# Performance work log

Hardware: AMD Instinct MI355X
Metric: run time of the kernel (lower is better)

Reference implementation:

```python
import jax, jax.numpy as jnp
import numpy as np

B, S, D = 8, 2048, 512


def setup_inputs() -> dict:
    root = jax.random.key(0)
    kq, kk, kv, km = jax.random.split(root, 4)
    query = jax.random.normal(kq, (B, S, D), dtype=jnp.float32)
    key = jax.random.normal(kk, (B, S, D), dtype=jnp.float32)
    value = jax.random.normal(kv, (B, S, D), dtype=jnp.float32)
    # padding mask (batch, key_len): 1 = attend, 0 = masked. Force position 0
    # valid so no causal row is entirely masked (would yield NaN softmax).
    attention_mask = jax.random.randint(km, (B, S), 0, 2, dtype=jnp.int32).at[:, 0].set(1)
    return {"query": query, "key": key, "value": value, "attention_mask": attention_mask}


def reference(query, key, value, attention_mask):
    q_len, k_len = query.shape[1], key.shape[1]
    scale = 1.0 / jnp.sqrt(jnp.asarray(key.shape[-1], dtype=query.dtype))
    # [B, q_len, k_len] scores
    scores = jnp.einsum("bqd,bkd->bqk", query, key) * scale
    # causal (mask_future=True): lower-triangular allowed
    causal = jnp.tril(jnp.ones((q_len, k_len), dtype=bool))
    scores = jnp.where(causal[None, :, :], scores, -jnp.inf)
    # padding mask broadcast over query axis: (B, 1, k_len)
    scores = jnp.where(attention_mask[:, None, :] == 0, -jnp.inf, scores)
    probs = jax.nn.softmax(scores, axis=-1)
    return jnp.einsum("bqk,bkd->bqd", probs, value)
```

## Files before the change

### kernel.cpp

```cpp
#include <hip/hip_runtime.h>
#include <hip/hip_bf16.h>


typedef short bf16x8 __attribute__((ext_vector_type(8)));
typedef short s4v    __attribute__((ext_vector_type(4)));
typedef float f32x4  __attribute__((ext_vector_type(4)));
typedef float f4v    __attribute__((ext_vector_type(4)));
typedef float f2v    __attribute__((ext_vector_type(2)));
typedef unsigned int u32;

#define DEVINL __device__ __forceinline__

constexpr int kS = 2048;
constexpr int kD = 512;
constexpr int kB = 8;
constexpr int QT = 32;
constexpr int KROW = kD + 8;
constexpr float kC = 1.4426950408889634f * 0.044194173824159216f;
constexpr size_t kSlotB = (size_t)64 * kD * 2 + 64 * 4 * 2;

DEVINL float fast_exp2(float x) {
  float r; asm("v_exp_f32 %0, %1" : "=v"(r) : "v"(x)); return r;
}
DEVINL short f2b(float f) {
  return (short)__builtin_bit_cast(unsigned short, __float2bfloat16(f));
}
DEVINL f32x4 mfma16(bf16x8 a, bf16x8 b, f32x4 c) {
  return __builtin_amdgcn_mfma_f32_16x16x32_bf16(a, b, c, 0, 0, 0);
}
DEVINL void gl_lds16(const void* g, void* l) {
  __builtin_amdgcn_global_load_lds(
      (const __attribute__((address_space(1))) u32*)g,
      (__attribute__((address_space(3))) u32*)l, 16, 0, 0);
}
DEVINL float bflo(u32 u) { return __builtin_bit_cast(float, u << 16); }
DEVINL float bfhi(u32 u) { return __builtin_bit_cast(float, u & 0xffff0000u); }

DEVINL int ncOf(int qt, int TT) { return (2 * qt + 2 + TT - 1) / TT; }

__global__ __launch_bounds__(256) void prep(
    const float* __restrict__ K, const float* __restrict__ V,
    short* __restrict__ Kb, short* __restrict__ Vt) {
  __shared__ float Tl[64][65];
  const int blk = blockIdx.x;
  if (blk < 1024) {
    const size_t n4 = (size_t)kB * kS * kD / 4;
    for (size_t i = (size_t)blk * 256 + threadIdx.x; i < n4;
         i += (size_t)1024 * 256) {
      f4v v = *(const f4v*)(K + i * 4);
      s4v o = {f2b(v[0]), f2b(v[1]), f2b(v[2]), f2b(v[3])};
      *(s4v*)(Kb + i * 4) = o;
    }
  } else {
    const int r = blk - 1024;
    const int b = r >> 8, rr = r & 255;
    const int s0 = (rr >> 3) * 64, d0 = (rr & 7) * 64;
    const int t = threadIdx.x;
#pragma unroll
    for (int i = 0; i < 4; ++i) {
      int v = t + i * 256;
      int row = v >> 4, cq = v & 15;
      f4v x = *(const f4v*)(V + ((size_t)(b * kS + s0 + row)) * kD + d0 + cq * 4);
      *(f4v*)&Tl[row][cq * 4] = x;
    }
    __syncthreads();
    const int dd = t >> 2, q = t & 3;
    short out[16];
#pragma unroll
    for (int j = 0; j < 16; ++j) out[j] = f2b(Tl[q * 16 + j][dd]);
    short* dp = Vt + ((size_t)(b * kD + d0 + dd)) * kS + s0 + q * 16;
    *(bf16x8*)dp = *(const bf16x8*)&out[0];
    *(bf16x8*)(dp + 8) = *(const bf16x8*)&out[8];
  }
}

__global__ __launch_bounds__(256, 1) void attn_p1(
    const float* __restrict__ Qp, const short* __restrict__ Kb,
    const short* __restrict__ Vt, const int* __restrict__ Mp,
    float* __restrict__ Op, char* __restrict__ Part, int TT, int NS) {
  __shared__ __align__(16) short Klds[2][32 * 512];
  __shared__ __align__(16) short Vlds[2][128 * 128];
  __shared__ __align__(16) short Plds[4 * 16 * 40];
  __shared__ unsigned char Mlds[kS];

  const int tid = threadIdx.x, lane = tid & 63, w = tid >> 6;
  const int b = blockIdx.x & 7;
  const int NCH = gridDim.x >> 3;
  const int jj = NCH - 1 - (blockIdx.x >> 3);

  int rem = jj, qt = 0, sub = 0;
  for (qt = 0; qt < QT; ++qt) {
    int c = ncOf(qt, TT);
    if (rem < c) { sub = rem; break; }
    rem -= c;
  }
  const int nc = ncOf(qt, TT);
  const int ntl = 2 * qt + 2;
  const int clen = (ntl + nc - 1) / nc;
  const int t0 = sub * clen, t1 = min(ntl, t0 + clen);
  const int qbase = qt * 64;

  for (int i = tid; i < kS; i += 256) Mlds[i] = (unsigned char)Mp[(size_t)b * kS + i];
  __syncthreads();

  const int l15 = lane & 15, lg = lane >> 4;
  const short* kbG = Kb + (size_t)(b * kS) * kD;
  const short* vtG = Vt + (size_t)(b * kD) * kS;

  auto stage = [&](int t, int nb) {
    const int kv0 = t * 32;
    const short* kb = kbG + (size_t)kv0 * kD;
    const short* vt = vtG + kv0;
    const int li = lane & 15, lh = lane >> 4;
#pragma unroll
    for (int r8 = 0; r8 < 8; ++r8) {
      const int row = w * 8 + r8;
      gl_lds16(kb + (size_t)row * kD + ((lane ^ (row & 7)) << 3),
               &Klds[nb][row * 512]);
    }
#pragma unroll
    for (int r8 = 0; r8 < 8; ++r8) {
      const int i = w * 8 + r8;
      const int sr = 4 * i + lh;
      const int logical = li ^ (4 * (i & 1) + lh);
      const int d = sr * 4 + (logical >> 2);
      gl_lds16(vt + (size_t)d * kS + ((logical & 3) << 3), &Vlds[nb][i * 512]);
    }
  };

  stage(t0, 0);

  bf16x8 qa[16];
  {
    const float* qp = Qp + ((size_t)(b * kS) + qbase + w * 16 + l15) * kD + lg * 8;
#pragma unroll
    for (int k = 0; k < 16; ++k) {
      f4v a = *(const f4v*)(qp + k * 32);
      f4v c = *(const f4v*)(qp + k * 32 + 4);
      bf16x8 q8 = {f2b(a[0]), f2b(a[1]), f2b(a[2]), f2b(a[3]),
                   f2b(c[0]), f2b(c[1]), f2b(c[2]), f2b(c[3])};
      qa[k] = q8;
    }
  }

  f32x4 acc[32];
#pragma unroll
  for (int dc = 0; dc < 32; ++dc) acc[dc] = f32x4{0.f, 0.f, 0.f, 0.f};
  float mrow[4] = {-1e30f, -1e30f, -1e30f, -1e30f};
  float lsum[4] = {0.f, 0.f, 0.f, 0.f};

  short* Pl = &Plds[w * 16 * 40];

  const int kx4 = (l15 >> 2) & 1;
  const int kcom = l15 * 512 + ((lg ^ (l15 & 3)) << 3);
  const int kEo = kcom + (kx4 << 5);
  const int kOo = kcom - (kx4 << 5);
  const int vcom = (l15 >> 2) * 128 + ((l15 >> 1) & 1) * 64 + ((lg ^ (l15 >> 2)) << 3);
  const int vEo = vcom + (l15 & 1) * 32;
  const int vOo = vcom + ((l15 & 1) ^ 1) * 32;

  for (int t = t0; t < t1; ++t) {
    const int cur = (t - t0) & 1;
    const int kv0 = t * 32;

    if (t + 1 < t1) {
      stage(t + 1, cur ^ 1);
      asm volatile("s_waitcnt vmcnt(16)" ::: "memory");
    } else {
      asm volatile("s_waitcnt vmcnt(0)" ::: "memory");
    }
    __builtin_amdgcn_s_barrier();
    __builtin_amdgcn_sched_barrier(0);

    const short* KB_ = &Klds[cur][0];
    const short* VB_ = &Vlds[cur][0];
    const short* kpE = KB_ + kEo;
    const short* kpO = KB_ + kOo;

    f32x4 sA = {0.f,0.f,0.f,0.f}, sB = {0.f,0.f,0.f,0.f};
    f32x4 sC = {0.f,0.f,0.f,0.f}, sD = {0.f,0.f,0.f,0.f};
    __builtin_amdgcn_s_setprio(1);
#pragma unroll
    for (int k = 0; k < 16; k += 2) {
      const short* pa = kpE + (k << 5);
      const short* pb = kpO + ((k + 1) << 5);
      bf16x8 b00 = *(const bf16x8*)(pa);
      bf16x8 b10 = *(const bf16x8*)(pa + 16 * 512);
      bf16x8 b01 = *(const bf16x8*)(pb);
      bf16x8 b11 = *(const bf16x8*)(pb + 16 * 512);
      sA = mfma16(qa[k], b00, sA);
      sB = mfma16(qa[k], b10, sB);
      sC = mfma16(qa[k + 1], b01, sC);
      sD = mfma16(qa[k + 1], b11, sD);
    }
    __builtin_amdgcn_s_setprio(0);
    f32x4 s0 = sA + sC;
    f32x4 s1 = sB + sD;

    const int kvg0 = kv0 + l15, kvg1 = kvg0 + 16;
    const int mk0 = Mlds[kvg0], mk1 = Mlds[kvg1];
    const int qrow0 = qbase + w * 16 + lg * 4;
    float rm[4];
#pragma unroll
    for (int jx = 0; jx < 4; ++jx) {
      const int q = qrow0 + jx;
      float x0 = (kvg0 <= q && mk0 != 0) ? s0[jx] : -1e30f;
      float x1 = (kvg1 <= q && mk1 != 0) ? s1[jx] : -1e30f;
      s0[jx] = x0; s1[jx] = x1;
      rm[jx] = fmaxf(x0, x1);
    }
#pragma unroll
    for (int sh = 1; sh <= 8; sh <<= 1) {
#pragma unroll
      for (int jx = 0; jx < 4; ++jx) rm[jx] = fmaxf(rm[jx], __shfl_xor(rm[jx], sh));
    }

    bool need = false;
#pragma unroll
    for (int jx = 0; jx < 4; ++jx) need |= ((rm[jx] - mrow[jx]) * kC > 8.0f);
    if (__any(need)) {
#pragma unroll
      for (int jx = 0; jx < 4; ++jx) {
        float mn = fmaxf(mrow[jx], rm[jx]);
        float corr = fast_exp2((mrow[jx] - mn) * kC);
        mrow[jx] = mn;
        lsum[jx] *= corr;
#pragma unroll
        for (int dc = 0; dc < 32; ++dc) acc[dc][jx] *= corr;
      }
    }

    float ts[4];
#pragma unroll
    for (int jx = 0; jx < 4; ++jx) {
      float p0 = fast_exp2((s0[jx] - mrow[jx]) * kC);
      float p1 = fast_exp2((s1[jx] - mrow[jx]) * kC);
      ts[jx] = p0 + p1;
      Pl[(lg * 4 + jx) * 40 + l15]      = f2b(p0);
      Pl[(lg * 4 + jx) * 40 + 16 + l15] = f2b(p1);
    }
#pragma unroll
    for (int sh = 1; sh <= 8; sh <<= 1) {
#pragma unroll
      for (int jx = 0; jx < 4; ++jx) ts[jx] += __shfl_xor(ts[jx], sh);
    }
#pragma unroll
    for (int jx = 0; jx < 4; ++jx) lsum[jx] += ts[jx];

    bf16x8 pf = *(const bf16x8*)&Pl[l15 * 40 + lg * 8];
    __builtin_amdgcn_s_setprio(1);
#pragma unroll
    for (int dc = 0; dc < 32; dc += 2) {
      bf16x8 vf0 = *(const bf16x8*)(VB_ + vEo + dc * 512);
      bf16x8 vf1 = *(const bf16x8*)(VB_ + vOo + (dc + 1) * 512);
      acc[dc]     = mfma16(pf, vf0, acc[dc]);
      acc[dc + 1] = mfma16(pf, vf1, acc[dc + 1]);
    }
    __builtin_amdgcn_s_setprio(0);

    __builtin_amdgcn_s_barrier();
  }

  if (nc == 1) {
#pragma unroll
    for (int jx = 0; jx < 4; ++jx) {
      const float inv = __builtin_amdgcn_rcpf(lsum[jx]);
      float* op = Op + ((size_t)(b * kS) + qbase + w * 16 + lg * 4 + jx) * kD + l15;
#pragma unroll
      for (int dc = 0; dc < 32; ++dc) op[dc * 16] = acc[dc][jx] * inv;
    }
  } else {
    int sb = 0;
    for (int q = 0; q < qt; ++q) {
      int n2 = ncOf(q, TT);
      if (n2 > 1) sb += n2;
    }
    char* sp = Part + ((size_t)b * NS + sb + sub) * kSlotB;
    short* po = (short*)sp;
    float* pm = (float*)(sp + 65536);
#pragma unroll
    for (int jx = 0; jx < 4; ++jx) {
      const int row = w * 16 + lg * 4 + jx;
#pragma unroll
      for (int dc = 0; dc < 32; ++dc) po[row * kD + dc * 16 + l15] = f2b(acc[dc][jx]);
      if (l15 == 0) { pm[row] = mrow[jx]; pm[64 + row] = lsum[jx]; }
    }
  }
}

__global__ __launch_bounds__(256) void attn_p2(const char* __restrict__ Part,
                                               float* __restrict__ Op,
                                               int TT, int NS) {
  const int bid = blockIdx.x;
  const int b = bid & 7, rg = (bid >> 3) & 7, idx = bid >> 6;
  int seen = 0, qt = 0, nc = 0, sbase = 0, sb = 0;
  for (int q = 0; q < QT; ++q) {
    int n2 = ncOf(q, TT);
    if (n2 > 1) {
      if (seen == idx) { qt = q; nc = n2; sbase = sb; break; }
      seen++;
      sb += n2;
    }
  }
  const int t = threadIdx.x;
  const char* base = Part + ((size_t)b * NS + sbase) * kSlotB;
  const int r0 = rg * 8;
  for (int row = r0; row < r0 + 8; ++row) {
    float M = -1e30f;
    for (int c = 0; c < nc; ++c)
      M = fmaxf(M, *(const float*)(base + c * kSlotB + 65536 + row * 4));
    float lt = 0.f;
    for (int c = 0; c < nc; ++c) {
      float mc = *(const float*)(base + c * kSlotB + 65536 + row * 4);
      float lc = *(const float*)(base + c * kSlotB + 65536 + 256 + row * 4);
      lt += lc * fast_exp2((mc - M) * kC);
    }
    const float inv = 1.0f / lt;
    float a0 = 0.f, a1 = 0.f;
    for (int c = 0; c < nc; ++c) {
      float mc = *(const float*)(base + c * kSlotB + 65536 + row * 4);
      float e = fast_exp2((mc - M) * kC);
      u32 u = *(const u32*)(base + c * kSlotB + ((size_t)row * kD + t * 2) * 2);
      a0 += e * bflo(u);
      a1 += e * bfhi(u);
    }
    f2v o = {a0 * inv, a1 * inv};
    *(f2v*)(Op + ((size_t)(b * kS) + qt * 64 + row) * kD + t * 2) = o;
  }
}

__global__ __launch_bounds__(256) void attn_legacy(
    const float* __restrict__ Qp, const float* __restrict__ Kp,
    const float* __restrict__ Vp, const int* __restrict__ Mp,
    float* __restrict__ Op) {
  __shared__ __align__(16) short Klds[32 * KROW];
  __shared__ __align__(16) short Vlds[32 * kD];
  __shared__ __align__(16) short Plds[4 * 16 * 40];
  __shared__ int Mlds[kS];
  const int tid = threadIdx.x, lane = tid & 63, w = tid >> 6;
  const int bb = blockIdx.x & 7, qt = blockIdx.x >> 3, qb = qt * 64;
  for (int i = tid; i < kS; i += 256) Mlds[i] = Mp[(size_t)bb * kS + i];
  const int l15 = lane & 15, lg = lane >> 4;
  bf16x8 qa[16];
  {
    const float* qp = Qp + ((size_t)bb * kS + qb + w * 16 + l15) * kD + lg * 8;
#pragma unroll
    for (int k = 0; k < 16; ++k) {
      f4v a = *(const f4v*)(qp + k * 32);
      f4v c = *(const f4v*)(qp + k * 32 + 4);
      bf16x8 q8 = {f2b(a[0]), f2b(a[1]), f2b(a[2]), f2b(a[3]),
                   f2b(c[0]), f2b(c[1]), f2b(c[2]), f2b(c[3])};
      qa[k] = q8;
    }
  }
  f32x4 acc[32];
#pragma unroll
  for (int dc = 0; dc < 32; ++dc) acc[dc] = f32x4{0.f, 0.f, 0.f, 0.f};
  float mrow[4] = {-1e30f, -1e30f, -1e30f, -1e30f};
  float lsum[4] = {0.f, 0.f, 0.f, 0.f};
  short* Pl = &Plds[w * 16 * 40];
  const int vphys = ((lg ^ ((lane >> 2) & 3)) * 16);
  const int nt = 2 * qt + 2;
  for (int t = 0; t < nt; ++t) {
    const int kv0 = t * 32;
    __syncthreads();
    {
      const int r = tid >> 3, dg = tid & 7;
      const float* src = Kp + ((size_t)bb * kS + kv0 + r) * kD + dg * 64;
      short* dst = &Klds[r * KROW + dg * 64];
#pragma unroll
      for (int i = 0; i < 16; ++i) {
        f4v v = *(const f4v*)(src + i * 4);
        s4v s = {f2b(v[0]), f2b(v[1]), f2b(v[2]), f2b(v[3])};
        *(s4v*)(dst + i * 4) = s;
      }
    }
    {
      const int kvq = tid & 7, dqi = tid >> 3;
      const float* vbase = Vp + ((size_t)bb * kS + kv0 + kvq * 4) * kD;
#pragma unroll
      for (int it = 0; it < 4; ++it) {
        const int dq = dqi + 32 * it;
        f4v v0 = *(const f4v*)(vbase + 0 * kD + dq * 4);
        f4v v1 = *(const f4v*)(vbase + 1 * kD + dq * 4);
        f4v v2 = *(const f4v*)(vbase + 2 * kD + dq * 4);
        f4v v3 = *(const f4v*)(vbase + 3 * kD + dq * 4);
        const int pch = (((kvq >> 1) ^ (dq & 3)) * 16) + (kvq & 1) * 8;
#pragma unroll
        for (int c = 0; c < 4; ++c) {
          s4v s = {f2b(v0[c]), f2b(v1[c]), f2b(v2[c]), f2b(v3[c])};
          *(s4v*)((char*)Vlds + (dq * 4 + c) * 64 + pch) = s;
        }
      }
    }
    __syncthreads();
    f32x4 sA = {0.f,0.f,0.f,0.f}, sB = {0.f,0.f,0.f,0.f};
    f32x4 sC = {0.f,0.f,0.f,0.f}, sD = {0.f,0.f,0.f,0.f};
    const short* krow0 = &Klds[l15 * KROW + lg * 8];
    const short* krow1 = krow0 + 16 * KROW;
#pragma unroll
    for (int k = 0; k < 16; k += 2) {
      bf16x8 b00 = *(const bf16x8*)(krow0 + k * 32);
      bf16x8 b10 = *(const bf16x8*)(krow1 + k * 32);
      bf16x8 b01 = *(const bf16x8*)(krow0 + (k + 1) * 32);
      bf16x8 b11 = *(const bf16x8*)(krow1 + (k + 1) * 32);
      sA = mfma16(qa[k], b00, sA);
      sB = mfma16(qa[k], b10, sB);
      sC = mfma16(qa[k + 1], b01, sC);
      sD = mfma16(qa[k + 1], b11, sD);
    }
    f32x4 s0 = sA + sC, s1 = sB + sD;
    const int kvg0 = kv0 + l15, kvg1 = kvg0 + 16;
    const int mk0 = Mlds[kvg0], mk1 = Mlds[kvg1];
    const int qrow0 = qb + w * 16 + lg * 4;
    float rm[4];
#pragma unroll
    for (int jx = 0; jx < 4; ++jx) {
      const int q = qrow0 + jx;
      float x0 = (kvg0 <= q && mk0 != 0) ? s0[jx] : -1e30f;
      float x1 = (kvg1 <= q && mk1 != 0) ? s1[jx] : -1e30f;
      s0[jx] = x0; s1[jx] = x1;
      rm[jx] = fmaxf(x0, x1);
    }
#pragma unroll
    for (int sh = 1; sh <= 8; sh <<= 1) {
#pragma unroll
      for (int jx = 0; jx < 4; ++jx) rm[jx] = fmaxf(rm[jx], __shfl_xor(rm[jx], sh));
    }
    bool need = false;
#pragma unroll
    for (int jx = 0; jx < 4; ++jx) need |= ((rm[jx] - mrow[jx]) * kC > 8.0f);
    if (__any(need)) {
#pragma unroll
      for (int jx = 0; jx < 4; ++jx) {
        float mn = fmaxf(mrow[jx], rm[jx]);
        float corr = fast_exp2((mrow[jx] - mn) * kC);
        mrow[jx] = mn;
        lsum[jx] *= corr;
#pragma unroll
        for (int dc = 0; dc < 32; ++dc) acc[dc][jx] *= corr;
      }
    }
    float ts[4];
#pragma unroll
    for (int jx = 0; jx < 4; ++jx) {
      float p0 = fast_exp2((s0[jx] - mrow[jx]) * kC);
      float p1 = fast_exp2((s1[jx] - mrow[jx]) * kC);
      ts[jx] = p0 + p1;
      Pl[(lg * 4 + jx) * 40 + l15]      = f2b(p0);
      Pl[(lg * 4 + jx) * 40 + 16 + l15] = f2b(p1);
    }
#pragma unroll
    for (int sh = 1; sh <= 8; sh <<= 1) {
#pragma unroll
      for (int jx = 0; jx < 4; ++jx) ts[jx] += __shfl_xor(ts[jx], sh);
    }
#pragma unroll
    for (int jx = 0; jx < 4; ++jx) lsum[jx] += ts[jx];
    bf16x8 pf = *(const bf16x8*)&Pl[l15 * 40 + lg * 8];
#pragma unroll
    for (int dc = 0; dc < 32; ++dc) {
      const bf16x8 vf = *(const bf16x8*)((const char*)Vlds + (dc * 16 + l15) * 64 + vphys);
      acc[dc] = mfma16(pf, vf, acc[dc]);
    }
  }
#pragma unroll
  for (int jx = 0; jx < 4; ++jx) {
    const float inv = __builtin_amdgcn_rcpf(lsum[jx]);
    float* op = Op + ((size_t)bb * kS + qb + w * 16 + lg * 4 + jx) * kD + l15;
#pragma unroll
    for (int dc = 0; dc < 32; ++dc) op[dc * 16] = acc[dc][jx] * inv;
  }
}

extern "C" void kernel_launch(void* const* d_in, const int* in_sizes, int n_in,
                              void* d_out, int out_size, void* d_ws, size_t ws_size,
                              hipStream_t stream) {
  const float* Q = (const float*)d_in[0];
  const float* K = (const float*)d_in[1];
  const float* V = (const float*)d_in[2];
  const int*   M = (const int*)d_in[3];
  float* O = (float*)d_out;

  const size_t tens = (size_t)kB * kS * kD;
  const size_t convB = 2 * tens * 2;

  if (ws_size < convB) {
    attn_legacy<<<dim3(256), dim3(256), 0, stream>>>(Q, K, V, M, O);
    return;
  }

  short* Kb = (short*)d_ws;
  short* Vt = Kb + tens;
  char* Part = (char*)d_ws + convB;
  const size_t budget = ws_size - convB;

  int TT = 64;
  {
    const int cands[4] = {16, 22, 33, 48};
    for (int ci = 0; ci < 4; ++ci) {
      int tt = cands[ci], slots = 0;
      for (int q = 0; q < QT; ++q) {
        int nc = (2 * q + 2 + tt - 1) / tt;
        if (nc > 1) slots += nc;
      }
      if ((size_t)kB * slots * kSlotB <= budget) { TT = tt; break; }
    }
  }
  int NS = 0, NCH = 0, nsplit = 0;
  for (int q = 0; q < QT; ++q) {
    int nc = (2 * q + 2 + TT - 1) / TT;
    NCH += nc;
    if (nc > 1) { NS += nc; nsplit++; }
  }

  prep<<<dim3(3072), dim3(256), 0, stream>>>(K, V, Kb, Vt);
  attn_p1<<<dim3(kB * NCH), dim3(256), 0, stream>>>(Q, Kb, Vt, M, O, Part, TT, NS);
  if (nsplit > 0)
    attn_p2<<<dim3(kB * 8 * nsplit), dim3(256), 0, stream>>>(Part, O, TT, NS);
}
```

Measured before the change: 216.2 us.

## Double query tile to 128 rows with 8 waves sharing staged K/V tiles

Each attention block now covers 128 query rows with 512 threads (8 waves), so every staged K/V tile in LDS is reused by twice as many query rows and global-to-LDS traffic per query row is halved. The split-K chunking, partial-slot layout and combine kernel are resized to the new tile. Row max and row sum reductions switch from shuffle loops to DPP row moves. The trade-off is fewer, larger blocks with higher register pressure at two blocks per CU, plus coarser causal load balance.

```diff
diff --git a/kernel.cpp b/kernel.cpp
--- a/kernel.cpp
+++ b/kernel.cpp
@@ -14,10 +14,11 @@
 constexpr int kS = 2048;
 constexpr int kD = 512;
 constexpr int kB = 8;
-constexpr int QT = 32;
+constexpr int QT2 = 16;
 constexpr int KROW = kD + 8;
 constexpr float kC = 1.4426950408889634f * 0.044194173824159216f;
-constexpr size_t kSlotB = (size_t)64 * kD * 2 + 64 * 4 * 2;
+constexpr int kPOff = 128 * kD * 2;
+constexpr size_t kSlot2 = (size_t)kPOff + 128 * 4 * 2;
 
 DEVINL float fast_exp2(float x) {
   float r; asm("v_exp_f32 %0, %1" : "=v"(r) : "v"(x)); return r;
@@ -36,7 +37,29 @@
 DEVINL float bflo(u32 u) { return __builtin_bit_cast(float, u << 16); }
 DEVINL float bfhi(u32 u) { return __builtin_bit_cast(float, u & 0xffff0000u); }
 
-DEVINL int ncOf(int qt, int TT) { return (2 * qt + 2 + TT - 1) / TT; }
+template <int CTRL>
+DEVINL float mvdpp(float x) {
+  return __builtin_bit_cast(float,
+      __builtin_amdgcn_mov_dpp(__builtin_bit_cast(int, x), CTRL, 0xf, 0xf, false));
+}
+DEVINL float rowmax16(float x) {
+  x = fmaxf(x, mvdpp<0x128>(x));
+  x = fmaxf(x, mvdpp<0x124>(x));
+  x = fmaxf(x, mvdpp<0x122>(x));
+  x = fmaxf(x, mvdpp<0x121>(x));
+  return x;
+}
+DEVINL float rowsum16(float x) {
+  x += mvdpp<0x128>(x);
+  x += mvdpp<0x124>(x);
+  x += mvdpp<0x122>(x);
+  x += mvdpp<0x121>(x);
+  return x;
+}
+
+__host__ __device__ __forceinline__ int nc2(int q, int TT) {
+  return (4 * q + 4 + TT - 1) / TT;
+}
 
 __global__ __launch_bounds__(256) void prep(
     const float* __restrict__ K, const float* __restrict__ V,
@@ -74,13 +97,13 @@
   }
 }
 
-__global__ __launch_bounds__(256, 1) void attn_p1(
+__global__ __launch_bounds__(512, 2) void attn_p1(
     const float* __restrict__ Qp, const short* __restrict__ Kb,
     const short* __restrict__ Vt, const int* __restrict__ Mp,
     float* __restrict__ Op, char* __restrict__ Part, int TT, int NS) {
   __shared__ __align__(16) short Klds[2][32 * 512];
   __shared__ __align__(16) short Vlds[2][128 * 128];
-  __shared__ __align__(16) short Plds[4 * 16 * 40];
+  __shared__ __align__(16) short Plds[8 * 16 * 40];
   __shared__ unsigned char Mlds[kS];
 
   const int tid = threadIdx.x, lane = tid & 63, w = tid >> 6;
@@ -89,18 +112,18 @@
   const int jj = NCH - 1 - (blockIdx.x >> 3);
 
   int rem = jj, qt = 0, sub = 0;
-  for (qt = 0; qt < QT; ++qt) {
-    int c = ncOf(qt, TT);
+  for (qt = 0; qt < QT2; ++qt) {
+    int c = nc2(qt, TT);
     if (rem < c) { sub = rem; break; }
     rem -= c;
   }
-  const int nc = ncOf(qt, TT);
-  const int ntl = 2 * qt + 2;
+  const int nc = nc2(qt, TT);
+  const int ntl = 4 * qt + 4;
   const int clen = (ntl + nc - 1) / nc;
   const int t0 = sub * clen, t1 = min(ntl, t0 + clen);
-  const int qbase = qt * 64;
-
-  for (int i = tid; i < kS; i += 256) Mlds[i] = (unsigned char)Mp[(size_t)b * kS + i];
+  const int qbase = qt * 128;
+
+  for (int i = tid; i < kS; i += 512) Mlds[i] = (unsigned char)Mp[(size_t)b * kS + i];
   __syncthreads();
 
   const int l15 = lane & 15, lg = lane >> 4;
@@ -113,14 +136,14 @@
     const short* vt = vtG + kv0;
     const int li = lane & 15, lh = lane >> 4;
 #pragma unroll
-    for (int r8 = 0; r8 < 8; ++r8) {
-      const int row = w * 8 + r8;
+    for (int r8 = 0; r8 < 4; ++r8) {
+      const int row = w * 4 + r8;
       gl_lds16(kb + (size_t)row * kD + ((lane ^ (row & 7)) << 3),
                &Klds[nb][row * 512]);
     }
 #pragma unroll
-    for (int r8 = 0; r8 < 8; ++r8) {
-      const int i = w * 8 + r8;
+    for (int r8 = 0; r8 < 4; ++r8) {
+      const int i = w * 4 + r8;
       const int sr = 4 * i + lh;
       const int logical = li ^ (4 * (i & 1) + lh);
       const int d = sr * 4 + (logical >> 2);
@@ -165,7 +188,7 @@
 
     if (t + 1 < t1) {
       stage(t + 1, cur ^ 1);
-      asm volatile("s_waitcnt vmcnt(16)" ::: "memory");
+      asm volatile("s_waitcnt vmcnt(8)" ::: "memory");
     } else {
       asm volatile("s_waitcnt vmcnt(0)" ::: "memory");
     }
@@ -207,12 +230,7 @@
       float x0 = (kvg0 <= q && mk0 != 0) ? s0[jx] : -1e30f;
       float x1 = (kvg1 <= q && mk1 != 0) ? s1[jx] : -1e30f;
       s0[jx] = x0; s1[jx] = x1;
-      rm[jx] = fmaxf(x0, x1);
-    }
-#pragma unroll
-    for (int sh = 1; sh <= 8; sh <<= 1) {
-#pragma unroll
-      for (int jx = 0; jx < 4; ++jx) rm[jx] = fmaxf(rm[jx], __shfl_xor(rm[jx], sh));
+      rm[jx] = rowmax16(fmaxf(x0, x1));
     }
 
     bool need = false;
@@ -230,22 +248,14 @@
       }
     }
 
-    float ts[4];
 #pragma unroll
     for (int jx = 0; jx < 4; ++jx) {
       float p0 = fast_exp2((s0[jx] - mrow[jx]) * kC);
       float p1 = fast_exp2((s1[jx] - mrow[jx]) * kC);
-      ts[jx] = p0 + p1;
+      lsum[jx] += rowsum16(p0 + p1);
       Pl[(lg * 4 + jx) * 40 + l15]      = f2b(p0);
       Pl[(lg * 4 + jx) * 40 + 16 + l15] = f2b(p1);
     }
-#pragma unroll
-    for (int sh = 1; sh <= 8; sh <<= 1) {
-#pragma unroll
-      for (int jx = 0; jx < 4; ++jx) ts[jx] += __shfl_xor(ts[jx], sh);
-    }
-#pragma unroll
-    for (int jx = 0; jx < 4; ++jx) lsum[jx] += ts[jx];
 
     bf16x8 pf = *(const bf16x8*)&Pl[l15 * 40 + lg * 8];
     __builtin_amdgcn_s_setprio(1);
@@ -272,18 +282,18 @@
   } else {
     int sb = 0;
     for (int q = 0; q < qt; ++q) {
-      int n2 = ncOf(q, TT);
+      int n2 = nc2(q, TT);
       if (n2 > 1) sb += n2;
     }
-    char* sp = Part + ((size_t)b * NS + sb + sub) * kSlotB;
+    char* sp = Part + ((size_t)b * NS + sb + sub) * kSlot2;
     short* po = (short*)sp;
-    float* pm = (float*)(sp + 65536);
+    float* pm = (float*)(sp + kPOff);
 #pragma unroll
     for (int jx = 0; jx < 4; ++jx) {
       const int row = w * 16 + lg * 4 + jx;
 #pragma unroll
       for (int dc = 0; dc < 32; ++dc) po[row * kD + dc * 16 + l15] = f2b(acc[dc][jx]);
-      if (l15 == 0) { pm[row] = mrow[jx]; pm[64 + row] = lsum[jx]; }
+      if (l15 == 0) { pm[row] = mrow[jx]; pm[128 + row] = lsum[jx]; }
     }
   }
 }
@@ -292,10 +302,10 @@
                                                float* __restrict__ Op,
                                                int TT, int NS) {
   const int bid = blockIdx.x;
-  const int b = bid & 7, rg = (bid >> 3) & 7, idx = bid >> 6;
+  const int b = bid & 7, rg = (bid >> 3) & 15, idx = bid >> 7;
   int seen = 0, qt = 0, nc = 0, sbase = 0, sb = 0;
-  for (int q = 0; q < QT; ++q) {
-    int n2 = ncOf(q, TT);
+  for (int q = 0; q < QT2; ++q) {
+    int n2 = nc2(q, TT);
     if (n2 > 1) {
       if (seen == idx) { qt = q; nc = n2; sbase = sb; break; }
       seen++;
@@ -303,29 +313,29 @@
     }
   }
   const int t = threadIdx.x;
-  const char* base = Part + ((size_t)b * NS + sbase) * kSlotB;
+  const char* base = Part + ((size_t)b * NS + sbase) * kSlot2;
   const int r0 = rg * 8;
   for (int row = r0; row < r0 + 8; ++row) {
     float M = -1e30f;
     for (int c = 0; c < nc; ++c)
-      M = fmaxf(M, *(const float*)(base + c * kSlotB + 65536 + row * 4));
+      M = fmaxf(M, *(const float*)(base + c * kSlot2 + kPOff + row * 4));
     float lt = 0.f;
     for (int c = 0; c < nc; ++c) {
-      float mc = *(const float*)(base + c * kSlotB + 65536 + row * 4);
-      float lc = *(const float*)(base + c * kSlotB + 65536 + 256 + row * 4);
+      float mc = *(const float*)(base + c * kSlot2 + kPOff + row * 4);
+      float lc = *(const float*)(base + c * kSlot2 + kPOff + 512 + row * 4);
       lt += lc * fast_exp2((mc - M) * kC);
     }
     const float inv = 1.0f / lt;
     float a0 = 0.f, a1 = 0.f;
     for (int c = 0; c < nc; ++c) {
-      float mc = *(const float*)(base + c * kSlotB + 65536 + row * 4);
+      float mc = *(const float*)(base + c * kSlot2 + kPOff + row * 4);
       float e = fast_exp2((mc - M) * kC);
-      u32 u = *(const u32*)(base + c * kSlotB + ((size_t)row * kD + t * 2) * 2);
+      u32 u = *(const u32*)(base + c * kSlot2 + ((size_t)row * kD + t * 2) * 2);
       a0 += e * bflo(u);
       a1 += e * bfhi(u);
     }
     f2v o = {a0 * inv, a1 * inv};
-    *(f2v*)(Op + ((size_t)(b * kS) + qt * 64 + row) * kD + t * 2) = o;
+    *(f2v*)(Op + ((size_t)(b * kS) + qt * 128 + row) * kD + t * 2) = o;
   }
 }
 
@@ -495,27 +505,27 @@
   char* Part = (char*)d_ws + convB;
   const size_t budget = ws_size - convB;
 
-  int TT = 64;
+  int TT = 68;
   {
-    const int cands[4] = {16, 22, 33, 48};
-    for (int ci = 0; ci < 4; ++ci) {
+    const int cands[5] = {8, 12, 16, 24, 34};
+    for (int ci = 0; ci < 5; ++ci) {
       int tt = cands[ci], slots = 0;
-      for (int q = 0; q < QT; ++q) {
-        int nc = (2 * q + 2 + tt - 1) / tt;
+      for (int q = 0; q < QT2; ++q) {
+        int nc = nc2(q, tt);
         if (nc > 1) slots += nc;
       }
-      if ((size_t)kB * slots * kSlotB <= budget) { TT = tt; break; }
+      if ((size_t)kB * slots * kSlot2 <= budget) { TT = tt; break; }
     }
   }
   int NS = 0, NCH = 0, nsplit = 0;
-  for (int q = 0; q < QT; ++q) {
-    int nc = (2 * q + 2 + TT - 1) / TT;
+  for (int q = 0; q < QT2; ++q) {
+    int nc = nc2(q, TT);
     NCH += nc;
     if (nc > 1) { NS += nc; nsplit++; }
   }
 
   prep<<<dim3(3072), dim3(256), 0, stream>>>(K, V, Kb, Vt);
-  attn_p1<<<dim3(kB * NCH), dim3(256), 0, stream>>>(Q, Kb, Vt, M, O, Part, TT, NS);
+  attn_p1<<<dim3(kB * NCH), dim3(512), 0, stream>>>(Q, Kb, Vt, M, O, Part, TT, NS);
   if (nsplit > 0)
-    attn_p2<<<dim3(kB * 8 * nsplit), dim3(256), 0, stream>>>(Part, O, TT, NS);
-}
+    attn_p2<<<dim3(kB * 16 * nsplit), dim3(256), 0, stream>>>(Part, O, TT, NS);
+}
```

New measurement: 195.8 us. -9.4%, faster.
